# Performance work log

Measured on AMD Instinct MI355X. Metric: run time of the kernel, lower is better.

Reference implementation:

```python
import jax, jax.numpy as jnp
import numpy as np

WS = (2, 7, 7)          # window size (Wd, Wh, Ww)
SS = (1, 3, 3)          # shift size
DIM = 96
HEADS = 3
HD = DIM // HEADS       # head dim = 32
N = WS[0] * WS[1] * WS[2]  # 98 tokens per window
EPS = 1e-5


def _rel_index():
    c = np.stack(np.meshgrid(np.arange(WS[0]), np.arange(WS[1]), np.arange(WS[2]), indexing='ij')).reshape(3, -1)
    r = (c[:, :, None] - c[:, None, :]).transpose(1, 2, 0)  # (N, N, 3)
    r[..., 0] += WS[0] - 1
    r[..., 1] += WS[1] - 1
    r[..., 2] += WS[2] - 1
    r[..., 0] *= (2 * WS[1] - 1) * (2 * WS[2] - 1)
    r[..., 1] *= 2 * WS[2] - 1
    return jnp.asarray(r.sum(-1))  # (N, N) int

REL_IDX = _rel_index()


def _ln(x, w, b):
    m = x.mean(-1, keepdims=True)
    v = ((x - m) ** 2).mean(-1, keepdims=True)
    return (x - m) * jax.lax.rsqrt(v + EPS) * w + b


def setup_inputs() -> dict:
    key = jax.random.key(0)
    ks = jax.random.split(key, 10)
    B, D, H, W, C = 2, 16, 112, 112, DIM
    nW = (D // WS[0]) * (H // WS[1]) * (W // WS[2])  # 2048
    s = 0.02
    tbl = (2 * WS[0] - 1) * (2 * WS[1] - 1) * (2 * WS[2] - 1)
    return dict(
        x=jax.random.normal(ks[0], (B, D, H, W, C), jnp.float32),
        mask=jax.random.normal(ks[1], (nW, N, N), jnp.float32),
        norm1_w=jnp.ones((C,), jnp.float32), norm1_b=jnp.zeros((C,), jnp.float32),
        qkv_w=jax.random.normal(ks[2], (C, 3 * C), jnp.float32) * s,
        qkv_b=jnp.zeros((3 * C,), jnp.float32),
        rpb_table=jax.random.normal(ks[3], (tbl, HEADS), jnp.float32) * s,
        proj_w=jax.random.normal(ks[4], (C, C), jnp.float32) * s,
        proj_b=jnp.zeros((C,), jnp.float32),
        norm2_w=jnp.ones((C,), jnp.float32), norm2_b=jnp.zeros((C,), jnp.float32),
        fc1_w=jax.random.normal(ks[5], (C, 4 * C), jnp.float32) * s,
        fc1_b=jnp.zeros((4 * C,), jnp.float32),
        fc2_w=jax.random.normal(ks[6], (4 * C, C), jnp.float32) * s,
        fc2_b=jnp.zeros((C,), jnp.float32),
    )


def reference(x, mask, norm1_w, norm1_b, qkv_w, qkv_b, rpb_table, proj_w, proj_b,
              norm2_w, norm2_b, fc1_w, fc1_b, fc2_w, fc2_b):
    B, D, H, W, C = x.shape
    shortcut = x
    x = _ln(x, norm1_w, norm1_b)
    # shift (dims divisible by window -> no padding needed)
    x = jnp.roll(x, shift=(-SS[0], -SS[1], -SS[2]), axis=(1, 2, 3))
    nd, nh, nw = D // WS[0], H // WS[1], W // WS[2]
    # window partition -> (B*nW, N, C)
    xw = x.reshape(B, nd, WS[0], nh, WS[1], nw, WS[2], C)
    xw = xw.transpose(0, 1, 3, 5, 2, 4, 6, 7).reshape(-1, N, C)
    B_ = xw.shape[0]
    qkv = (xw @ qkv_w + qkv_b).reshape(B_, N, 3, HEADS, HD).transpose(2, 0, 3, 1, 4)
    q, k, v = qkv[0] * (HD ** -0.5), qkv[1], qkv[2]
    attn = jnp.einsum('bhnd,bhmd->bhnm', q, k)  # (B_, H, N, N)
    bias = rpb_table[REL_IDX.reshape(-1)].reshape(N, N, HEADS).transpose(2, 0, 1)
    attn = attn + bias[None]
    nWm = mask.shape[0]
    attn = attn.reshape(B_ // nWm, nWm, HEADS, N, N) + mask[None, :, None]
    attn = jax.nn.softmax(attn.reshape(B_, HEADS, N, N), axis=-1)
    out = jnp.einsum('bhnm,bhmd->bhnd', attn, v).transpose(0, 2, 1, 3).reshape(B_, N, C)
    out = out @ proj_w + proj_b
    # window reverse
    x = out.reshape(B, nd, nh, nw, WS[0], WS[1], WS[2], C)
    x = x.transpose(0, 1, 4, 2, 5, 3, 6, 7).reshape(B, D, H, W, C)
    x = jnp.roll(x, shift=SS, axis=(1, 2, 3))
    x = shortcut + x
    y = _ln(x, norm2_w, norm2_b)
    y = jax.nn.gelu(y @ fc1_w + fc1_b, approximate=False) @ fc2_w + fc2_b
    return x + y
```

## Files before the change

kernel.cpp:

```cpp
#include <hip/hip_runtime.h>

typedef float f32x4 __attribute__((ext_vector_type(4)));
typedef __bf16 bf16x8 __attribute__((ext_vector_type(8)));
typedef unsigned short ushort_t;
typedef ushort_t us4 __attribute__((ext_vector_type(4)));
typedef unsigned int u32x4 __attribute__((ext_vector_type(4)));

#define MFMA16(a, b, c) __builtin_amdgcn_mfma_f32_16x16x32_bf16((a), (b), (c), 0, 0, 0)
#define LOG2E 1.4426950408889634f

__device__ __forceinline__ ushort_t f2bf(float f) {
    unsigned int u = __builtin_bit_cast(unsigned int, f);
    u += 0x7fffu + ((u >> 16) & 1u);
    return (ushort_t)(u >> 16);
}
__device__ __forceinline__ float bf2f(ushort_t u) {
    return __builtin_bit_cast(float, (unsigned int)u << 16);
}
__device__ __forceinline__ unsigned int packbf2(float lo, float hi) {
    return ((unsigned int)f2bf(hi) << 16) | (unsigned int)f2bf(lo);
}

__device__ __forceinline__ float gelu_fast(float x) {
    float x2 = x * x;
    float t = __builtin_fmaf(0.044715f * x2, x, x);
    float e = __builtin_amdgcn_exp2f(t * (-1.5957691216f * 1.44269504f));
    return x * __builtin_amdgcn_rcpf(1.0f + e);
}

#define NTOK 98
#define CCH 96
#define QSCALE 0.17677669529663687f

#define WQKVP_OFF   ((size_t)0)
#define WPROJP_OFF  (WQKVP_OFF + (size_t)27648 * 2)
#define WFC1P_OFF   (WPROJP_OFF + (size_t)9216 * 2)
#define WFC2P_OFF   (WFC1P_OFF + (size_t)36864 * 2)
#define BIAS2_OFF   (WFC2P_OFF + (size_t)36864 * 2)
#define MASK2_OFF   (BIAS2_OFF + (size_t)37632 * 2 + 256)

__global__ __launch_bounds__(256) void prep_kernel(
    const float* __restrict__ qkv_w, const float* __restrict__ proj_w,
    const float* __restrict__ fc1_w, const float* __restrict__ fc2_w,
    const float* __restrict__ rpb,
    ushort_t* __restrict__ wqkvP, ushort_t* __restrict__ wprojP,
    ushort_t* __restrict__ wfc1P, ushort_t* __restrict__ wfc2P,
    ushort_t* __restrict__ bias2)
{
    int i = blockIdx.x * 256 + threadIdx.x;
    if (i < 27648) {
        int f = i >> 9, r = i & 511, lane = r >> 3, m = r & 7;
        int k0 = f % 3, t = f / 3, nt = t % 2, t2 = t / 2, w = t2 % 3, h = t2 / 3;
        int row = k0 * 32 + (lane >> 4) * 8 + m;
        int col = w * 96 + h * 32 + nt * 16 + (lane & 15);
        wqkvP[i] = f2bf(qkv_w[row * 288 + col]);
        return;
    }
    i -= 27648;
    if (i < 9216) {
        int f = i >> 9, r = i & 511, lane = r >> 3, m = r & 7;
        int k0 = f % 3, nt = f / 3;
        int row = k0 * 32 + (lane >> 4) * 8 + m;
        int col = nt * 16 + (lane & 15);
        wprojP[i] = f2bf(proj_w[row * 96 + col]);
        return;
    }
    i -= 9216;
    if (i < 36864) {
        int f = i >> 9, r = i & 511, lane = r >> 3, m = r & 7;
        int k0 = f % 3, nt = f / 3;
        int row = k0 * 32 + (lane >> 4) * 8 + m;
        int col = nt * 16 + (lane & 15);
        wfc1P[i] = f2bf(fc1_w[row * 384 + col]);
        return;
    }
    i -= 36864;
    if (i < 36864) {
        int f = i >> 9, r = i & 511, lane = r >> 3, m = r & 7;
        int k0 = f % 12, nt = f / 12;
        int row = k0 * 32 + (lane >> 4) * 8 + m;
        int col = nt * 16 + (lane & 15);
        wfc2P[i] = f2bf(fc2_w[row * 96 + col]);
        return;
    }
    i -= 36864;
    if (i < 37632) {
        int h = i / 12544, rem = i % 12544;
        int mt = rem / 1792, rem2 = rem % 1792, kc = rem2 >> 4, r16 = rem2 & 15;
        int row = mt * 16 + r16;
        float v = 0.f;
        if (row < 98 && kc < 98) {
            int rd = row / 49 - kc / 49 + 1;
            int rh = (row % 49) / 7 - (kc % 49) / 7 + 6;
            int rw = row % 7 - kc % 7 + 6;
            v = rpb[((rd * 13 + rh) * 13 + rw) * 3 + h] * LOG2E;
        }
        bias2[i] = f2bf(v);
    }
}

__global__ __launch_bounds__(256) void mask2_kernel(
    const float* __restrict__ mask, ushort_t* __restrict__ mask2)
{
    __shared__ float m_lds[9604];
    const int wm = blockIdx.x;
    const float* mw = mask + (size_t)wm * 9604;
    for (int i = threadIdx.x; i < 9604; i += 256) m_lds[i] = mw[i];
    __syncthreads();
    ushort_t* out = mask2 + (size_t)wm * 12544;
    for (int g = threadIdx.x; g < 3136; g += 256) {
        int mt = g / 448, rem = g % 448, kc = rem >> 2, r4 = (rem & 3) * 4;
        us4 o;
        #pragma unroll
        for (int e = 0; e < 4; ++e) {
            int row = mt * 16 + r4 + e;
            float v = (row < 98 && kc < 98) ? m_lds[row * 98 + kc] * LOG2E : -1e30f;
            o[e] = f2bf(v);
        }
        *(us4*)(out + (size_t)g * 4) = o;
    }
}

__global__ __launch_bounds__(192, 3) void fused_attn(
    const float* __restrict__ x, const ushort_t* __restrict__ mask2,
    const float* __restrict__ n1w, const float* __restrict__ n1b,
    const float* __restrict__ qkv_b, const float* __restrict__ proj_b,
    const ushort_t* __restrict__ wqkvP, const ushort_t* __restrict__ wprojP,
    const ushort_t* __restrict__ bias2, float* __restrict__ dout)
{
    __shared__ ushort_t xw_lds[112 * 104];
    __shared__ ushort_t sc_all[3][2176];
    __shared__ int tokbase[112];

    const int tid  = threadIdx.x;
    const int lane = tid & 63;
    const int wave = tid >> 6;
    const int l16  = lane & 15, lg = lane >> 4;

    const int b  = blockIdx.x;
    const int wm = (b & 7) * 256 + ((b >> 3) >> 1);
    const int bb = (b >> 3) & 1;
    const int id_ = wm >> 8, ih = (wm >> 4) & 15, iw = wm & 15;

    if (tid < 98) {
        int td = tid / 49, r49 = tid - td * 49, th = r49 / 7, tw = r49 - th * 7;
        int od = (id_ * 2 + td + 1) & 15;
        int oh = ih * 7 + th + 3; if (oh >= 112) oh -= 112;
        int ow = iw * 7 + tw + 3; if (ow >= 112) ow -= 112;
        tokbase[tid] = ((((bb << 4) + od) * 112 + oh) * 112 + ow) * 96;
    }
    {
        us4 z4 = {0, 0, 0, 0};
        for (int i = tid; i < 14 * 26; i += 192) {
            int t = 98 + i / 26, c4 = (i % 26) * 4;
            *(us4*)(xw_lds + t * 104 + c4) = z4;
        }
    }
    __syncthreads();

    {
        const int g = tid >> 5, lane32 = tid & 31;
        for (int t = g; t < 98; t += 6) {
            const float* xp = x + tokbase[t];
            float v0 = xp[lane32], v1 = xp[lane32 + 32], v2 = xp[lane32 + 64];
            float s = v0 + v1 + v2, sq = v0 * v0 + v1 * v1 + v2 * v2;
            #pragma unroll
            for (int m = 1; m < 32; m <<= 1) { s += __shfl_xor(s, m); sq += __shfl_xor(sq, m); }
            float mean = s * (1.0f / 96.0f);
            float var = sq * (1.0f / 96.0f) - mean * mean;
            float rs = rsqrtf(var + 1e-5f);
            ushort_t* op = xw_lds + t * 104;
            op[lane32]      = f2bf((v0 - mean) * rs * n1w[lane32]      + n1b[lane32]);
            op[lane32 + 32] = f2bf((v1 - mean) * rs * n1w[lane32 + 32] + n1b[lane32 + 32]);
            op[lane32 + 64] = f2bf((v2 - mean) * rs * n1w[lane32 + 64] + n1b[lane32 + 64]);
        }
    }
    __syncthreads();

    const int h = wave;
    ushort_t* sc = sc_all[wave];
    const ushort_t* m2w = mask2 + (size_t)wm * 12544;
    const ushort_t* b2h = bias2 + (size_t)h * 12544;

    bf16x8 qf[7], kf[7], vf[2][4];

    #pragma unroll
    for (int which = 0; which < 2; ++which) {
        bf16x8 bw[2][3];
        float  bia[2];
        #pragma unroll
        for (int nt = 0; nt < 2; ++nt) {
            bia[nt] = qkv_b[which * 96 + h * 32 + nt * 16 + l16];
            #pragma unroll
            for (int k0 = 0; k0 < 3; ++k0)
                bw[nt][k0] = *(const bf16x8*)(wqkvP + ((((h * 3 + which) * 2 + nt) * 3 + k0) << 9) + lane * 8);
        }
        for (int mt = 0; mt < 7; ++mt) {
            const ushort_t* ap = xw_lds + (mt * 16 + l16) * 104 + lg * 8;
            bf16x8 a0 = *(const bf16x8*)(ap);
            bf16x8 a1 = *(const bf16x8*)(ap + 32);
            bf16x8 a2 = *(const bf16x8*)(ap + 64);
            #pragma unroll
            for (int nt = 0; nt < 2; ++nt) {
                f32x4 acc = {0.f, 0.f, 0.f, 0.f};
                acc = MFMA16(a0, bw[nt][0], acc);
                acc = MFMA16(a1, bw[nt][1], acc);
                acc = MFMA16(a2, bw[nt][2], acc);
                float scl = (which == 0) ? (QSCALE * LOG2E) : 1.0f;
                #pragma unroll
                for (int j = 0; j < 4; ++j)
                    sc[(lg * 4 + j) * 36 + nt * 16 + l16] = f2bf((acc[j] + bia[nt]) * scl);
            }
            if (which == 0) qf[mt] = *(const bf16x8*)(sc + l16 * 36 + lg * 8);
            else            kf[mt] = *(const bf16x8*)(sc + l16 * 36 + lg * 8);
        }
    }

    {
        bf16x8 bw[2][3];
        float  bia[2];
        #pragma unroll
        for (int nt = 0; nt < 2; ++nt) {
            bia[nt] = qkv_b[192 + h * 32 + nt * 16 + l16];
            #pragma unroll
            for (int k0 = 0; k0 < 3; ++k0)
                bw[nt][k0] = *(const bf16x8*)(wqkvP + ((((h * 3 + 2) * 2 + nt) * 3 + k0) << 9) + lane * 8);
        }
        #pragma unroll
        for (int k0 = 0; k0 < 4; ++k0) {
            unsigned int pkv[2][2][2];
            #pragma unroll
            for (int half = 0; half < 2; ++half) {
                int mtp = 2 * k0 + half;
                if (mtp < 7) {
                    const ushort_t* ap = xw_lds + (mtp * 16 + l16) * 104 + lg * 8;
                    bf16x8 a0 = *(const bf16x8*)(ap);
                    bf16x8 a1 = *(const bf16x8*)(ap + 32);
                    bf16x8 a2 = *(const bf16x8*)(ap + 64);
                    #pragma unroll
                    for (int nt2 = 0; nt2 < 2; ++nt2) {
                        f32x4 acc = {0.f, 0.f, 0.f, 0.f};
                        acc = MFMA16(a0, bw[nt2][0], acc);
                        acc = MFMA16(a1, bw[nt2][1], acc);
                        acc = MFMA16(a2, bw[nt2][2], acc);
                        pkv[half][nt2][0] = packbf2(acc[0] + bia[nt2], acc[1] + bia[nt2]);
                        pkv[half][nt2][1] = packbf2(acc[2] + bia[nt2], acc[3] + bia[nt2]);
                    }
                } else {
                    pkv[half][0][0] = pkv[half][0][1] = 0u;
                    pkv[half][1][0] = pkv[half][1][1] = 0u;
                }
            }
            #pragma unroll
            for (int nt2 = 0; nt2 < 2; ++nt2) {
                u32x4 w;
                #pragma unroll
                for (int e = 0; e < 4; ++e) {
                    int s = l16 + 16 * (2 * (lg & 1) + (e >> 1));
                    unsigned int t0 = (unsigned int)__shfl((int)pkv[0][nt2][e & 1], s, 64);
                    unsigned int t1 = (unsigned int)__shfl((int)pkv[1][nt2][e & 1], s, 64);
                    w[e] = (lg >> 1) ? t1 : t0;
                }
                vf[nt2][k0] = __builtin_bit_cast(bf16x8, w);
            }
        }
    }
    __syncthreads();

    ushort_t* out = xw_lds;

    if (lane < 32) {
        us4 z4 = {0, 0, 0, 0};
        *(us4*)(sc + (lane >> 1) * 136 + 112 + (lane & 1) * 8) = z4;
        *(us4*)(sc + (lane >> 1) * 136 + 116 + (lane & 1) * 8) = z4;
    }

    #pragma unroll
    for (int mt = 0; mt < 7; ++mt) {
        const ushort_t* m2t = m2w + mt * 1792;
        const ushort_t* b2t = b2h + mt * 1792;
        us4 mv[7];
        #pragma unroll
        for (int nt = 0; nt < 7; ++nt)
            mv[nt] = *(const us4*)(m2t + (nt * 16 + l16) * 16 + lg * 4);

        f32x4 sums = {0.f, 0.f, 0.f, 0.f};
        #pragma unroll
        for (int nt = 0; nt < 7; ++nt) {
            us4 bv = *(const us4*)(b2t + (nt * 16 + l16) * 16 + lg * 4);
            f32x4 z = {0.f, 0.f, 0.f, 0.f};
            f32x4 stv = MFMA16(qf[mt], kf[nt], z);
            #pragma unroll
            for (int j = 0; j < 4; ++j) {
                float e_ = __builtin_amdgcn_exp2f(stv[j] + bf2f(mv[nt][j]) + bf2f(bv[j]));
                sums[j] += e_;
                sc[(lg * 4 + j) * 136 + nt * 16 + l16] = f2bf(e_);
            }
        }
        f32x4 inv;
        #pragma unroll
        for (int j = 0; j < 4; ++j) {
            float s = sums[j];
            s += __shfl_xor(s, 1); s += __shfl_xor(s, 2);
            s += __shfl_xor(s, 4); s += __shfl_xor(s, 8);
            inv[j] = __builtin_amdgcn_rcpf(s);
        }
        bf16x8 pf[4];
        #pragma unroll
        for (int k0 = 0; k0 < 4; ++k0)
            pf[k0] = *(const bf16x8*)(sc + l16 * 136 + k0 * 32 + lg * 8);
        #pragma unroll
        for (int nt2 = 0; nt2 < 2; ++nt2) {
            f32x4 acc = {0.f, 0.f, 0.f, 0.f};
            #pragma unroll
            for (int k0 = 0; k0 < 4; ++k0) acc = MFMA16(pf[k0], vf[nt2][k0], acc);
            #pragma unroll
            for (int j = 0; j < 4; ++j) {
                int tok = mt * 16 + lg * 4 + j;
                if (tok < 98)
                    out[tok * 104 + h * 32 + nt2 * 16 + l16] = f2bf(acc[j] * inv[j]);
            }
        }
    }
    __syncthreads();

    for (int job = wave; job < 42; job += 3) {
        int mt = job / 6, nt = job % 6;
        int cg = nt * 16 + l16;
        f32x4 acc = {0.f, 0.f, 0.f, 0.f};
        #pragma unroll
        for (int k0 = 0; k0 < 3; ++k0) {
            bf16x8 ao = *(const bf16x8*)(out + (mt * 16 + l16) * 104 + k0 * 32 + lg * 8);
            bf16x8 bp = *(const bf16x8*)(wprojP + ((nt * 3 + k0) << 9) + lane * 8);
            acc = MFMA16(ao, bp, acc);
        }
        float pb = proj_b[cg];
        #pragma unroll
        for (int j = 0; j < 4; ++j) {
            int tok = mt * 16 + lg * 4 + j;
            if (tok < 98) {
                int g = tokbase[tok] + cg;
                dout[g] = x[g] + acc[j] + pb;
            }
        }
    }
}

__global__ __launch_bounds__(256, 5) void mlp_kernel(
    float* __restrict__ xres, const float* __restrict__ w2, const float* __restrict__ b2,
    const ushort_t* __restrict__ wfc1P, const float* __restrict__ fc1_b,
    const ushort_t* __restrict__ wfc2P, const float* __restrict__ fc2_b)
{
    __shared__ ushort_t A_ln[32 * 104];
    __shared__ ushort_t h_lds[32 * 392];
    const int tid = threadIdx.x;
    const int lane = tid & 63, wave = tid >> 6;
    const int l16 = lane & 15, lg = lane >> 4;
    const size_t t0 = (size_t)blockIdx.x * 32;

    {
        int t = tid >> 3, sub = tid & 7;
        const float* xp = xres + (t0 + t) * 96;
        f32x4 v[3];
        float s = 0.f, sq = 0.f;
        #pragma unroll
        for (int j4 = 0; j4 < 3; ++j4) {
            v[j4] = *(const f32x4*)(xp + (j4 * 8 + sub) * 4);
            #pragma unroll
            for (int e = 0; e < 4; ++e) { s += v[j4][e]; sq += v[j4][e] * v[j4][e]; }
        }
        s += __shfl_xor(s, 1); s += __shfl_xor(s, 2); s += __shfl_xor(s, 4);
        sq += __shfl_xor(sq, 1); sq += __shfl_xor(sq, 2); sq += __shfl_xor(sq, 4);
        float mean = s * (1.0f / 96.0f);
        float var = sq * (1.0f / 96.0f) - mean * mean;
        float rs = rsqrtf(var + 1e-5f);
        #pragma unroll
        for (int j4 = 0; j4 < 3; ++j4) {
            int c0 = (j4 * 8 + sub) * 4;
            us4 pk;
            #pragma unroll
            for (int e = 0; e < 4; ++e)
                pk[e] = f2bf((v[j4][e] - mean) * rs * w2[c0 + e] + b2[c0 + e]);
            *(us4*)(A_ln + t * 104 + c0) = pk;
        }
    }
    __syncthreads();

    for (int job = wave; job < 48; job += 4) {
        int mt = job / 24, nt = job % 24;
        int n = nt * 16 + l16;
        f32x4 acc = {0.f, 0.f, 0.f, 0.f};
        #pragma unroll
        for (int k0 = 0; k0 < 3; ++k0) {
            bf16x8 a  = *(const bf16x8*)(A_ln + (mt * 16 + l16) * 104 + k0 * 32 + lg * 8);
            bf16x8 bw = *(const bf16x8*)(wfc1P + ((nt * 3 + k0) << 9) + lane * 8);
            acc = MFMA16(a, bw, acc);
        }
        float bv = fc1_b[n];
        #pragma unroll
        for (int j = 0; j < 4; ++j) {
            int tok = mt * 16 + lg * 4 + j;
            h_lds[tok * 392 + n] = f2bf(gelu_fast(acc[j] + bv));
        }
    }
    __syncthreads();

    for (int job = wave; job < 12; job += 4) {
        int mt = job / 6, nt = job % 6;
        int c = nt * 16 + l16;
        f32x4 acc = {0.f, 0.f, 0.f, 0.f};
        #pragma unroll
        for (int k0 = 0; k0 < 12; ++k0) {
            bf16x8 a  = *(const bf16x8*)(h_lds + (mt * 16 + l16) * 392 + k0 * 32 + lg * 8);
            bf16x8 bw = *(const bf16x8*)(wfc2P + ((nt * 12 + k0) << 9) + lane * 8);
            acc = MFMA16(a, bw, acc);
        }
        float bv = fc2_b[c];
        #pragma unroll
        for (int j = 0; j < 4; ++j) {
            int tok = mt * 16 + lg * 4 + j;
            size_t g = (t0 + tok) * 96 + c;
            xres[g] = xres[g] + acc[j] + bv;
        }
    }
}

extern "C" void kernel_launch(void* const* d_in, const int* in_sizes, int n_in,
                              void* d_out, int out_size, void* d_ws, size_t ws_size,
                              hipStream_t stream) {
    const float* x      = (const float*)d_in[0];
    const float* mask   = (const float*)d_in[1];
    const float* n1w    = (const float*)d_in[2];
    const float* n1b    = (const float*)d_in[3];
    const float* qkv_w  = (const float*)d_in[4];
    const float* qkv_b  = (const float*)d_in[5];
    const float* rpb    = (const float*)d_in[6];
    const float* proj_w = (const float*)d_in[7];
    const float* proj_b = (const float*)d_in[8];
    const float* n2w    = (const float*)d_in[9];
    const float* n2b    = (const float*)d_in[10];
    const float* fc1_w  = (const float*)d_in[11];
    const float* fc1_b  = (const float*)d_in[12];
    const float* fc2_w  = (const float*)d_in[13];
    const float* fc2_b  = (const float*)d_in[14];

    char* ws = (char*)d_ws;
    ushort_t* wqkvP  = (ushort_t*)(ws + WQKVP_OFF);
    ushort_t* wprojP = (ushort_t*)(ws + WPROJP_OFF);
    ushort_t* wfc1P  = (ushort_t*)(ws + WFC1P_OFF);
    ushort_t* wfc2P  = (ushort_t*)(ws + WFC2P_OFF);
    ushort_t* bias2  = (ushort_t*)(ws + BIAS2_OFF);
    ushort_t* mask2  = (ushort_t*)(ws + MASK2_OFF);
    float*    dout   = (float*)d_out;

    prep_kernel<<<579, 256, 0, stream>>>(qkv_w, proj_w, fc1_w, fc2_w, rpb,
                                         wqkvP, wprojP, wfc1P, wfc2P, bias2);
    mask2_kernel<<<2048, 256, 0, stream>>>(mask, mask2);
    fused_attn<<<4096, 192, 0, stream>>>(x, mask2, n1w, n1b, qkv_b, proj_b,
                                         wqkvP, wprojP, bias2, dout);
    mlp_kernel<<<12544, 256, 0, stream>>>(dout, n2w, n2b, wfc1P, fc1_b, wfc2P, fc2_b);
}
```

Before: 497.3 us.

## Split attention query rows across two waves per head in fused_attn

Doubles the block to 384 threads (6 waves), so each head gets two waves and each wave handles about half of the query row tiles (4 or 3 of 7). Each wave computes only its own Q tiles, but both waves still compute the full K and V for their head. The aim is more parallelism and latency hiding per window, at the cost of duplicated K/V projection work and more LDS per block, which may lower occupancy.

```diff
diff --git a/kernel.cpp b/kernel.cpp
--- a/kernel.cpp
+++ b/kernel.cpp
@@ -121,7 +121,7 @@
     }
 }
 
-__global__ __launch_bounds__(192, 3) void fused_attn(
+__global__ __launch_bounds__(384, 3) void fused_attn(
     const float* __restrict__ x, const ushort_t* __restrict__ mask2,
     const float* __restrict__ n1w, const float* __restrict__ n1b,
     const float* __restrict__ qkv_b, const float* __restrict__ proj_b,
@@ -129,12 +129,16 @@
     const ushort_t* __restrict__ bias2, float* __restrict__ dout)
 {
     __shared__ ushort_t xw_lds[112 * 104];
-    __shared__ ushort_t sc_all[3][2176];
+    __shared__ ushort_t sc_all[6][2176];
     __shared__ int tokbase[112];
 
     const int tid  = threadIdx.x;
     const int lane = tid & 63;
     const int wave = tid >> 6;
+    const int h    = wave % 3;
+    const int half = wave / 3;
+    const int mt0  = half * 4;
+    const int mcnt = half ? 3 : 4;
     const int l16  = lane & 15, lg = lane >> 4;
 
     const int b  = blockIdx.x;
@@ -151,7 +155,7 @@
     }
     {
         us4 z4 = {0, 0, 0, 0};
-        for (int i = tid; i < 14 * 26; i += 192) {
+        for (int i = tid; i < 14 * 26; i += 384) {
             int t = 98 + i / 26, c4 = (i % 26) * 4;
             *(us4*)(xw_lds + t * 104 + c4) = z4;
         }
@@ -160,7 +164,7 @@
 
     {
         const int g = tid >> 5, lane32 = tid & 31;
-        for (int t = g; t < 98; t += 6) {
+        for (int t = g; t < 98; t += 12) {
             const float* xp = x + tokbase[t];
             float v0 = xp[lane32], v1 = xp[lane32 + 32], v2 = xp[lane32 + 64];
             float s = v0 + v1 + v2, sq = v0 * v0 + v1 * v1 + v2 * v2;
@@ -177,23 +181,52 @@
     }
     __syncthreads();
 
-    const int h = wave;
     ushort_t* sc = sc_all[wave];
     const ushort_t* m2w = mask2 + (size_t)wm * 12544;
     const ushort_t* b2h = bias2 + (size_t)h * 12544;
 
-    bf16x8 qf[7], kf[7], vf[2][4];
-
-    #pragma unroll
-    for (int which = 0; which < 2; ++which) {
+    bf16x8 qf[4], kf[7], vf[2][4];
+
+    {
         bf16x8 bw[2][3];
         float  bia[2];
         #pragma unroll
         for (int nt = 0; nt < 2; ++nt) {
-            bia[nt] = qkv_b[which * 96 + h * 32 + nt * 16 + l16];
+            bia[nt] = qkv_b[h * 32 + nt * 16 + l16];
             #pragma unroll
             for (int k0 = 0; k0 < 3; ++k0)
-                bw[nt][k0] = *(const bf16x8*)(wqkvP + ((((h * 3 + which) * 2 + nt) * 3 + k0) << 9) + lane * 8);
+                bw[nt][k0] = *(const bf16x8*)(wqkvP + (((h * 6 + nt) * 3 + k0) << 9) + lane * 8);
+        }
+        #pragma unroll
+        for (int i = 0; i < 4; ++i) if (i < mcnt) {
+            int mt = mt0 + i;
+            const ushort_t* ap = xw_lds + (mt * 16 + l16) * 104 + lg * 8;
+            bf16x8 a0 = *(const bf16x8*)(ap);
+            bf16x8 a1 = *(const bf16x8*)(ap + 32);
+            bf16x8 a2 = *(const bf16x8*)(ap + 64);
+            #pragma unroll
+            for (int nt = 0; nt < 2; ++nt) {
+                f32x4 acc = {0.f, 0.f, 0.f, 0.f};
+                acc = MFMA16(a0, bw[nt][0], acc);
+                acc = MFMA16(a1, bw[nt][1], acc);
+                acc = MFMA16(a2, bw[nt][2], acc);
+                #pragma unroll
+                for (int j = 0; j < 4; ++j)
+                    sc[(lg * 4 + j) * 36 + nt * 16 + l16] = f2bf((acc[j] + bia[nt]) * (QSCALE * LOG2E));
+            }
+            qf[i] = *(const bf16x8*)(sc + l16 * 36 + lg * 8);
+        }
+    }
+
+    {
+        bf16x8 bw[2][3];
+        float  bia[2];
+        #pragma unroll
+        for (int nt = 0; nt < 2; ++nt) {
+            bia[nt] = qkv_b[96 + h * 32 + nt * 16 + l16];
+            #pragma unroll
+            for (int k0 = 0; k0 < 3; ++k0)
+                bw[nt][k0] = *(const bf16x8*)(wqkvP + ((((h * 3 + 1) * 2 + nt) * 3 + k0) << 9) + lane * 8);
         }
         for (int mt = 0; mt < 7; ++mt) {
             const ushort_t* ap = xw_lds + (mt * 16 + l16) * 104 + lg * 8;
@@ -206,13 +239,11 @@
                 acc = MFMA16(a0, bw[nt][0], acc);
                 acc = MFMA16(a1, bw[nt][1], acc);
                 acc = MFMA16(a2, bw[nt][2], acc);
-                float scl = (which == 0) ? (QSCALE * LOG2E) : 1.0f;
                 #pragma unroll
                 for (int j = 0; j < 4; ++j)
-                    sc[(lg * 4 + j) * 36 + nt * 16 + l16] = f2bf((acc[j] + bia[nt]) * scl);
-            }
-            if (which == 0) qf[mt] = *(const bf16x8*)(sc + l16 * 36 + lg * 8);
-            else            kf[mt] = *(const bf16x8*)(sc + l16 * 36 + lg * 8);
+                    sc[(lg * 4 + j) * 36 + nt * 16 + l16] = f2bf(acc[j] + bia[nt]);
+            }
+            kf[mt] = *(const bf16x8*)(sc + l16 * 36 + lg * 8);
         }
     }
 
@@ -230,8 +261,8 @@
         for (int k0 = 0; k0 < 4; ++k0) {
             unsigned int pkv[2][2][2];
             #pragma unroll
-            for (int half = 0; half < 2; ++half) {
-                int mtp = 2 * k0 + half;
+            for (int half2 = 0; half2 < 2; ++half2) {
+                int mtp = 2 * k0 + half2;
                 if (mtp < 7) {
                     const ushort_t* ap = xw_lds + (mtp * 16 + l16) * 104 + lg * 8;
                     bf16x8 a0 = *(const bf16x8*)(ap);
@@ -243,12 +274,12 @@
                         acc = MFMA16(a0, bw[nt2][0], acc);
                         acc = MFMA16(a1, bw[nt2][1], acc);
                         acc = MFMA16(a2, bw[nt2][2], acc);
-                        pkv[half][nt2][0] = packbf2(acc[0] + bia[nt2], acc[1] + bia[nt2]);
-                        pkv[half][nt2][1] = packbf2(acc[2] + bia[nt2], acc[3] + bia[nt2]);
+                        pkv[half2][nt2][0] = packbf2(acc[0] + bia[nt2], acc[1] + bia[nt2]);
+                        pkv[half2][nt2][1] = packbf2(acc[2] + bia[nt2], acc[3] + bia[nt2]);
                     }
                 } else {
-                    pkv[half][0][0] = pkv[half][0][1] = 0u;
-                    pkv[half][1][0] = pkv[half][1][1] = 0u;
+                    pkv[half2][0][0] = pkv[half2][0][1] = 0u;
+                    pkv[half2][1][0] = pkv[half2][1][1] = 0u;
                 }
             }
             #pragma unroll
@@ -276,7 +307,8 @@
     }
 
     #pragma unroll
-    for (int mt = 0; mt < 7; ++mt) {
+    for (int i = 0; i < 4; ++i) if (i < mcnt) {
+        int mt = mt0 + i;
         const ushort_t* m2t = m2w + mt * 1792;
         const ushort_t* b2t = b2h + mt * 1792;
         us4 mv[7];
@@ -289,7 +321,7 @@
         for (int nt = 0; nt < 7; ++nt) {
             us4 bv = *(const us4*)(b2t + (nt * 16 + l16) * 16 + lg * 4);
             f32x4 z = {0.f, 0.f, 0.f, 0.f};
-            f32x4 stv = MFMA16(qf[mt], kf[nt], z);
+            f32x4 stv = MFMA16(qf[i], kf[nt], z);
             #pragma unroll
             for (int j = 0; j < 4; ++j) {
                 float e_ = __builtin_amdgcn_exp2f(stv[j] + bf2f(mv[nt][j]) + bf2f(bv[j]));
@@ -324,7 +356,7 @@
     }
     __syncthreads();
 
-    for (int job = wave; job < 42; job += 3) {
+    for (int job = wave; job < 42; job += 6) {
         int mt = job / 6, nt = job % 6;
         int cg = nt * 16 + l16;
         f32x4 acc = {0.f, 0.f, 0.f, 0.f};
@@ -456,7 +488,7 @@
     prep_kernel<<<579, 256, 0, stream>>>(qkv_w, proj_w, fc1_w, fc2_w, rpb,
                                          wqkvP, wprojP, wfc1P, wfc2P, bias2);
     mask2_kernel<<<2048, 256, 0, stream>>>(mask, mask2);
-    fused_attn<<<4096, 192, 0, stream>>>(x, mask2, n1w, n1b, qkv_b, proj_b,
+    fused_attn<<<4096, 384, 0, stream>>>(x, mask2, n1w, n1b, qkv_b, proj_b,
                                          wqkvP, wprojP, bias2, dout);
     mlp_kernel<<<12544, 256, 0, stream>>>(dout, n2w, n2b, wfc1P, fc1_b, wfc2P, fc2_b);
 }
```

After: 630.4 us. +26.8%, slower.
